# Performance work log

Measured on AMD Instinct MI355X. Metric: run time of the kernel, lower is better.

The kernel has to match this reference:

```python
import jax, jax.numpy as jnp
import numpy as np

B, S, D = 2, 1024, 1024
G, H = 8, 2
HD = D // (G * H)          # 64
E, TOPK, FF = 8, 2, 4 * D  # experts, active experts, ffn hidden
ROPE_THETA = 10000.0


def setup_inputs() -> dict:
    key = jax.random.key(0)
    ks = jax.random.split(key, 9)
    s = 0.02
    return {
        "x": jax.random.normal(ks[0], (B, S, D), jnp.float32),
        "norm1_w": jnp.ones((D,), jnp.float32),
        "Wq": jax.random.normal(ks[1], (G, D, H * HD), jnp.float32) * s,
        "Wk": jax.random.normal(ks[2], (G, D, HD), jnp.float32) * s,
        "Wv": jax.random.normal(ks[3], (G, D, HD), jnp.float32) * s,
        "norm2_w": jnp.ones((D,), jnp.float32),
        "router_w": jax.random.normal(ks[4], (D, E), jnp.float32) * s,
        "w_gate": jax.random.normal(ks[5], (E, D, FF), jnp.float32) * s,
        "w_up": jax.random.normal(ks[6], (E, D, FF), jnp.float32) * s,
        "w_down": jax.random.normal(ks[7], (E, FF, D), jnp.float32) * s,
    }


def rmsnorm(x, w, eps=1e-6):
    var = jnp.mean(x * x, axis=-1, keepdims=True)
    return w * (x * jax.lax.rsqrt(var + eps))


def rope_cos_sin(seq, hd, dtype):
    inv = 1.0 / (ROPE_THETA ** (jnp.arange(0, hd, 2, dtype=jnp.float32) / hd))
    ang = jnp.arange(seq, dtype=jnp.float32)[:, None] * inv  # [S, hd/2]
    return jnp.cos(ang).astype(dtype), jnp.sin(ang).astype(dtype)


def apply_rope(x, cos, sin):
    x1, x2 = jnp.split(x, 2, axis=-1)
    return jnp.concatenate([x1 * cos - x2 * sin, x1 * sin + x2 * cos], axis=-1)


def reference(x, norm1_w, Wq, Wk, Wv, norm2_w, router_w, w_gate, w_up, w_down):
    b, s, d = x.shape
    g, hd = Wk.shape[0], Wk.shape[-1]
    h_per_g = Wq.shape[-1] // hd
    e = router_w.shape[-1]

    # --- norm1 + grouped RoPE attention (H query heads share 1 KV per group) ---
    hx = rmsnorm(x, norm1_w)
    q = jnp.einsum('bsd,gdm->bgsm', hx, Wq).reshape(b, g, s, h_per_g, hd)
    q = q.transpose(0, 1, 3, 2, 4)                      # [b,g,h,s,hd]
    k = jnp.einsum('bsd,gde->bgse', hx, Wk)             # [b,g,s,hd]
    v = jnp.einsum('bsd,gde->bgse', hx, Wv)
    cos, sin = rope_cos_sin(s, hd, x.dtype)
    q = apply_rope(q, cos, sin)
    k = apply_rope(k, cos, sin)
    scores = jnp.einsum('bghsd,bgtd->bghst', q, k) / jnp.asarray(np.sqrt(hd), x.dtype)
    causal = jnp.tril(jnp.ones((s, s), bool))
    scores = jnp.where(causal, scores, jnp.finfo(x.dtype).min)
    attn = jax.nn.softmax(scores, axis=-1)
    o = jnp.einsum('bghst,bgtd->bghsd', attn, v)
    attn_out = o.transpose(0, 3, 1, 2, 4).reshape(b, s, d)  # concat groups, then heads
    x1 = x + attn_out

    # --- norm2 + MoE (top-k softmax router, SwiGLU experts) ---
    h2 = rmsnorm(x1, norm2_w)
    probs = jax.nn.softmax(h2 @ router_w, axis=-1)       # [b,s,E]
    topv, topi = jax.lax.top_k(probs, TOPK)
    topv = topv / jnp.sum(topv, axis=-1, keepdims=True)  # renormalize active weights
    onehot = jax.nn.one_hot(topi, e, dtype=x.dtype)      # [b,s,K,E]
    gates = jnp.einsum('bsk,bske->bse', topv, onehot)    # dense gate per expert

    moe_out = jnp.zeros_like(h2)
    for ei in range(e):  # small fixed expert count
        act = jax.nn.silu(h2 @ w_gate[ei]) * (h2 @ w_up[ei])
        moe_out = moe_out + gates[..., ei:ei + 1] * (act @ w_down[ei])

    # Switch/Mixtral load-balancing loss
    f = jnp.mean(onehot, axis=(0, 1, 2))   # fraction of assignments per expert
    p = jnp.mean(probs, axis=(0, 1))       # mean router prob per expert
    aux = jnp.asarray(e, x.dtype) * jnp.sum(f * p)

    return x1 + moe_out, aux
```

## Files before the change

### kernel.cpp

```cpp
#include <hip/hip_runtime.h>
#include <hip/hip_bf16.h>

typedef __hip_bfloat16 bf16;

#define BB 2
#define SS 1024
#define DD 1024
#define GG 8
#define HH 2
#define HDIM 64
#define EE 8
#define KTOP 2
#define FFD 4096
#define NTOK (BB*SS)
#define NSEL (NTOK*KTOP)

typedef __attribute__((ext_vector_type(8))) short bf16x8v;
typedef __attribute__((ext_vector_type(4))) float f32x4;
typedef __attribute__((ext_vector_type(4))) unsigned int u32x4;

union FragU { uint32_t u[4]; bf16x8v v; };
union FragQ { u32x4 q; bf16x8v v; };

__device__ __forceinline__ float b2f(bf16 v){ return __bfloat162float(v); }
__device__ __forceinline__ bf16  f2b(float v){ return __float2bfloat16(v); }
__device__ __forceinline__ uint32_t f2bu(float f){
  union { bf16 b; unsigned short u; } c; c.b = __float2bfloat16(f); return (uint32_t)c.u;
}
__device__ __forceinline__ uint32_t packbf(float lo, float hi){
  return f2bu(lo) | (f2bu(hi) << 16);
}

__global__ void rmsnorm_kernel(const float* __restrict__ x, const float* __restrict__ w,
                               float* __restrict__ out){
  int row = blockIdx.x, tid = threadIdx.x;
  const float* xr = x + (size_t)row * DD;
  float v0 = xr[tid];
  float v1 = xr[tid+256];
  float v2 = xr[tid+512];
  float v3 = xr[tid+768];
  float ss = v0*v0+v1*v1+v2*v2+v3*v3;
  for (int off=32; off; off>>=1) ss += __shfl_down(ss, off);
  __shared__ float red[4];
  if ((tid&63)==0) red[tid>>6]=ss;
  __syncthreads();
  float inv = rsqrtf((red[0]+red[1]+red[2]+red[3])*(1.0f/DD) + 1e-6f);
  float* orow = out + (size_t)row*DD;
  orow[tid]     = v0*inv*w[tid];
  orow[tid+256] = v1*inv*w[tid+256];
  orow[tid+512] = v2*inv*w[tid+512];
  orow[tid+768] = v3*inv*w[tid+768];
}

__global__ void rmsnorm_b16_kernel(const float* __restrict__ x, const float* __restrict__ w,
                                   bf16* __restrict__ out){
  int row = blockIdx.x, tid = threadIdx.x;
  const float* xr = x + (size_t)row * DD;
  float v0 = xr[tid];
  float v1 = xr[tid+256];
  float v2 = xr[tid+512];
  float v3 = xr[tid+768];
  float ss = v0*v0+v1*v1+v2*v2+v3*v3;
  for (int off=32; off; off>>=1) ss += __shfl_down(ss, off);
  __shared__ float red[4];
  if ((tid&63)==0) red[tid>>6]=ss;
  __syncthreads();
  float inv = rsqrtf((red[0]+red[1]+red[2]+red[3])*(1.0f/DD) + 1e-6f);
  bf16* orow = out + (size_t)row*DD;
  orow[tid]     = f2b(v0*inv*w[tid]);
  orow[tid+256] = f2b(v1*inv*w[tid+256]);
  orow[tid+512] = f2b(v2*inv*w[tid+512]);
  orow[tid+768] = f2b(v3*inv*w[tid+768]);
}

__global__ void __launch_bounds__(256) qkv_mfma(const bf16* __restrict__ hxb,
      const float* __restrict__ Wq, const float* __restrict__ Wk, const float* __restrict__ Wv,
      float* __restrict__ q, float* __restrict__ k, bf16* __restrict__ vb){
  int mtile = blockIdx.x;
  int nt = blockIdx.y;
  int g = nt >> 2, sub = nt & 3;
  const float* wsrc; int ld;
  if (sub < 2){ wsrc = Wq + (size_t)g*DD*128 + sub*64; ld = 128; }
  else if (sub == 2){ wsrc = Wk + (size_t)g*DD*64; ld = 64; }
  else { wsrc = Wv + (size_t)g*DD*64; ld = 64; }

  __shared__ __attribute__((aligned(16))) uint32_t Bt[64][20];
  int tid = threadIdx.x;
  int w = tid >> 6, l = tid & 63, lg = l >> 4, lr = l & 15;
  int wm = (w >> 1)*32, wn = (w & 1)*32;

  const bf16* arow[2];
  #pragma unroll
  for (int mf=0; mf<2; mf++)
    arow[mf] = hxb + (size_t)(mtile*64 + wm + mf*16 + lr)*DD;

  int scol = tid & 63, skp = tid >> 6;

  f32x4 acc[2][2];
  #pragma unroll
  for (int mf=0;mf<2;mf++)
    #pragma unroll
    for (int nf=0;nf<2;nf++) acc[mf][nf] = (f32x4){0,0,0,0};

  float gld[8];
  #pragma unroll
  for (int jj=0;jj<8;jj++) gld[jj] = wsrc[(size_t)(8*skp + jj)*ld + scol];

  for (int kb=0; kb<DD; kb+=32){
    __syncthreads();
    uint32_t pk[4];
    #pragma unroll
    for (int j2=0;j2<4;j2++) pk[j2] = packbf(gld[2*j2], gld[2*j2+1]);
    *(u32x4*)&Bt[scol][4*skp] = (u32x4){pk[0],pk[1],pk[2],pk[3]};
    __syncthreads();
    if (kb + 32 < DD){
      #pragma unroll
      for (int jj=0;jj<8;jj++) gld[jj] = wsrc[(size_t)(kb + 32 + 8*skp + jj)*ld + scol];
    }
    bf16x8v af[2];
    #pragma unroll
    for (int mf=0;mf<2;mf++)
      af[mf] = *(const bf16x8v*)(arow[mf] + kb + lg*8);
    #pragma unroll
    for (int nf=0;nf<2;nf++){
      FragQ bfr;
      bfr.q = *(const u32x4*)&Bt[wn + nf*16 + lr][lg*4];
      #pragma unroll
      for (int mf=0;mf<2;mf++)
        acc[mf][nf] = __builtin_amdgcn_mfma_f32_16x16x32_bf16(af[mf], bfr.v, acc[mf][nf], 0,0,0);
    }
  }
  #pragma unroll
  for (int mf=0;mf<2;mf++){
    #pragma unroll
    for (int nf=0;nf<2;nf++){
      #pragma unroll
      for (int r=0;r<4;r++){
        int token = mtile*64 + wm + mf*16 + lg*4 + r;
        int b = token >> 10, s = token & (SS-1);
        int c = wn + nf*16 + lr;
        float val = acc[mf][nf][r];
        if (sub < 2)       q[(((size_t)(b*GG+g)*HH + sub)*SS + s)*HDIM + c] = val;
        else if (sub == 2) k[(((size_t)(b*GG+g))*SS + s)*HDIM + c] = val;
        else               vb[(((size_t)(b*GG+g))*SS + s)*HDIM + c] = f2b(val);
      }
    }
  }
}

__global__ void rope_cast_kernel(const float* __restrict__ pin, bf16* __restrict__ pout, int nrows){
  int idx = blockIdx.x*256 + threadIdx.x;
  if (idx >= nrows*32) return;
  int r = idx >> 5, i = idx & 31;
  int s = r & (SS-1);
  float inv = expf(-9.210340371976184f * (float)i / 32.0f);
  float ang = (float)s * inv;
  float sn = sinf(ang), cs = cosf(ang);
  const float* row = pin + (size_t)r * HDIM;
  float a = row[i], b = row[i+32];
  pout[(size_t)r*HDIM + i]      = f2b(a*cs - b*sn);
  pout[(size_t)r*HDIM + i + 32] = f2b(a*sn + b*cs);
}

__global__ void __launch_bounds__(256) attn_mfma(
    const bf16* __restrict__ qb, const bf16* __restrict__ kb, const bf16* __restrict__ vb,
    const float* __restrict__ x, float* __restrict__ x1){
  int qt = blockIdx.x;
  int bh = blockIdx.y;
  int b = bh >> 4, gh = bh & 15;
  int bg = b*GG + (gh >> 1);
  int q0 = qt * 64;

  int tid = threadIdx.x;
  int w = tid >> 6, l = tid & 63, lg = l >> 4, lr = l & 15;

  __shared__ uint32_t Vp[32][68];
  __shared__ uint32_t Plu[4][16][33];

  const bf16* qbase = qb + ((size_t)bh*SS + q0 + w*16 + lr)*HDIM;
  bf16x8v qfr[2];
  qfr[0] = *(const bf16x8v*)(qbase + lg*8);
  qfr[1] = *(const bf16x8v*)(qbase + 32 + lg*8);

  f32x4 O[4];
  #pragma unroll
  for (int i=0;i<4;i++) O[i] = (f32x4){0,0,0,0};
  float mrow[4] = {-3e38f,-3e38f,-3e38f,-3e38f};
  float lrow[4] = {0.f,0.f,0.f,0.f};

  const bf16* kbg = kb + (size_t)bg*SS*HDIM;
  const unsigned short* vbg = (const unsigned short*)(vb + (size_t)bg*SS*HDIM);

  int c44 = (tid & 15)*4;
  int kpq = tid >> 4;

  for (int t=0; t<=qt; t++){
    int kv0 = t*64;
    __syncthreads();
    #pragma unroll
    for (int it=0; it<2; it++){
      int kp = kpq + it*16;
      const unsigned short* r0 = vbg + (size_t)(kv0 + 2*kp)*HDIM + c44;
      ushort4 a = *(const ushort4*)r0;
      ushort4 bq = *(const ushort4*)(r0 + HDIM);
      Vp[kp][c44+0] = (uint32_t)a.x | ((uint32_t)bq.x<<16);
      Vp[kp][c44+1] = (uint32_t)a.y | ((uint32_t)bq.y<<16);
      Vp[kp][c44+2] = (uint32_t)a.z | ((uint32_t)bq.z<<16);
      Vp[kp][c44+3] = (uint32_t)a.w | ((uint32_t)bq.w<<16);
    }
    __syncthreads();

    f32x4 sacc[4];
    #pragma unroll
    for (int nf=0;nf<4;nf++){
      sacc[nf] = (f32x4){0,0,0,0};
      const bf16* kr = kbg + (size_t)(kv0 + nf*16 + lr)*HDIM + lg*8;
      bf16x8v kf0 = *(const bf16x8v*)kr;
      bf16x8v kf1 = *(const bf16x8v*)(kr + 32);
      sacc[nf] = __builtin_amdgcn_mfma_f32_16x16x32_bf16(qfr[0], kf0, sacc[nf], 0,0,0);
      sacc[nf] = __builtin_amdgcn_mfma_f32_16x16x32_bf16(qfr[1], kf1, sacc[nf], 0,0,0);
    }

    bool diag = (t == qt);
    float p[4][4];
    float rmax[4] = {-3e38f,-3e38f,-3e38f,-3e38f};
    #pragma unroll
    for (int nf=0;nf<4;nf++){
      #pragma unroll
      for (int r=0;r<4;r++){
        float s = sacc[nf][r]*0.125f;
        if (diag && (nf*16+lr > w*16+lg*4+r)) s = -3e38f;
        p[nf][r] = s;
        rmax[r] = fmaxf(rmax[r], s);
      }
    }
    #pragma unroll
    for (int r=0;r<4;r++){
      #pragma unroll
      for (int mm=1; mm<16; mm<<=1) rmax[r] = fmaxf(rmax[r], __shfl_xor(rmax[r], mm));
      float mn = fmaxf(mrow[r], rmax[r]);
      float resc = __expf(mrow[r]-mn);
      mrow[r] = mn;
      float rsum = 0.f;
      #pragma unroll
      for (int nf=0;nf<4;nf++){
        float e = __expf(p[nf][r]-mn);
        p[nf][r] = e;
        rsum += e;
      }
      #pragma unroll
      for (int mm=1; mm<16; mm<<=1) rsum += __shfl_xor(rsum, mm);
      lrow[r] = lrow[r]*resc + rsum;
      O[0][r]*=resc; O[1][r]*=resc; O[2][r]*=resc; O[3][r]*=resc;
    }

    #pragma unroll
    for (int nf=0;nf<4;nf++){
      #pragma unroll
      for (int r=0;r<4;r++){
        float pnbr = __shfl_xor(p[nf][r], 1);
        if ((lr & 1) == 0)
          Plu[w][lg*4+r][(nf*16+lr)>>1] = packbf(p[nf][r], pnbr);
      }
    }

    #pragma unroll
    for (int kc=0;kc<2;kc++){
      FragU pa;
      #pragma unroll
      for (int jp=0;jp<4;jp++)
        pa.u[jp] = Plu[w][lr][kc*16 + lg*4 + jp];
      #pragma unroll
      for (int nf=0;nf<4;nf++){
        FragU vf;
        #pragma unroll
        for (int jp=0;jp<4;jp++) vf.u[jp] = Vp[kc*16 + lg*4 + jp][nf*16 + lr];
        O[nf] = __builtin_amdgcn_mfma_f32_16x16x32_bf16(pa.v, vf.v, O[nf], 0,0,0);
      }
    }
  }

  #pragma unroll
  for (int r=0;r<4;r++){
    int s = q0 + w*16 + lg*4 + r;
    float inv = 1.f/fmaxf(lrow[r], 1e-30f);
    size_t rowo = ((size_t)(b*SS + s))*DD + gh*HDIM;
    #pragma unroll
    for (int nf=0;nf<4;nf++){
      size_t oi = rowo + nf*16 + lr;
      x1[oi] = x[oi] + O[nf][r]*inv;
    }
  }
}

__global__ void router_kernel(const float* __restrict__ h2, const float* __restrict__ rw,
                              int* __restrict__ topi, float* __restrict__ topv,
                              float* __restrict__ probs){
  int token = blockIdx.x, tid = threadIdx.x;
  const float* hr = h2 + (size_t)token * DD;
  float part[EE];
  #pragma unroll
  for (int e=0;e<EE;e++) part[e]=0.f;
  for (int d = tid; d < DD; d += 256) {
    float hv = hr[d];
    #pragma unroll
    for (int e=0;e<EE;e++) part[e] += hv * rw[d*EE+e];
  }
  #pragma unroll
  for (int e=0;e<EE;e++)
    for (int off=32; off; off>>=1) part[e] += __shfl_down(part[e], off);
  __shared__ float red[4][EE];
  if ((tid&63)==0){
    #pragma unroll
    for (int e=0;e<EE;e++) red[tid>>6][e]=part[e];
  }
  __syncthreads();
  if (tid==0){
    float lg[EE];
    #pragma unroll
    for (int e=0;e<EE;e++) lg[e]=red[0][e]+red[1][e]+red[2][e]+red[3][e];
    float m = lg[0];
    #pragma unroll
    for (int e=1;e<EE;e++) m = fmaxf(m, lg[e]);
    float ex[EE], ssum=0.f;
    #pragma unroll
    for (int e=0;e<EE;e++){ ex[e]=expf(lg[e]-m); ssum+=ex[e]; }
    float p[EE];
    #pragma unroll
    for (int e=0;e<EE;e++){ p[e]=ex[e]/ssum; probs[token*EE+e]=p[e]; }
    int i1=0;
    for (int e=1;e<EE;e++) if (p[e]>p[i1]) i1=e;
    int i2=-1;
    for (int e=0;e<EE;e++) if (e!=i1 && (i2<0 || p[e]>p[i2])) i2=e;
    float g1=p[i1], g2=p[i2], gs=g1+g2;
    topi[token*2]=i1; topi[token*2+1]=i2;
    topv[token*2]=g1/gs; topv[token*2+1]=g2/gs;
  }
}

__global__ void stats_kernel(const float* __restrict__ probs, const int* __restrict__ topi,
                             float* __restrict__ sumP, int* __restrict__ counts){
  int tid = threadIdx.x;
  float ls[EE];
  int lc[EE];
  #pragma unroll
  for (int e=0;e<EE;e++){ ls[e]=0.f; lc[e]=0; }
  for (int t = tid; t < NTOK; t += 256){
    const float* pr = probs + (size_t)t*EE;
    #pragma unroll
    for (int e=0;e<EE;e++) ls[e] += pr[e];
    lc[topi[2*t]]++;
    lc[topi[2*t+1]]++;
  }
  #pragma unroll
  for (int e=0;e<EE;e++){
    for (int off=32; off; off>>=1){
      ls[e] += __shfl_down(ls[e], off);
      lc[e] += __shfl_down(lc[e], off);
    }
  }
  __shared__ float rs[4][EE];
  __shared__ int   rc[4][EE];
  if ((tid&63)==0){
    #pragma unroll
    for (int e=0;e<EE;e++){ rs[tid>>6][e]=ls[e]; rc[tid>>6][e]=lc[e]; }
  }
  __syncthreads();
  if (tid==0){
    #pragma unroll
    for (int e=0;e<EE;e++){
      sumP[e]   = rs[0][e]+rs[1][e]+rs[2][e]+rs[3][e];
      counts[e] = rc[0][e]+rc[1][e]+rc[2][e]+rc[3][e];
    }
  }
}

__global__ void fill_kernel(const int* __restrict__ topi, const float* __restrict__ topv,
                            const int* __restrict__ counts, int* __restrict__ offs,
                            int* __restrict__ tok_list, float* __restrict__ gate_list,
                            int* __restrict__ tdesc, int* __restrict__ ndesc){
  int tid = threadIdx.x;
  int w = tid >> 6, lane = tid & 63;
  if (tid < EE){
    int o = 0;
    for (int e=0;e<tid;e++) o += counts[e];
    offs[tid] = o;
  }
  if (tid == 0){
    int n = 0;
    for (int e=0;e<EE;e++){
      int t = (counts[e] + 255) >> 8;
      for (int m=0;m<t;m++) tdesc[n++] = e | (m << 8);
    }
    *ndesc = n;
  }
  int pos = 0;
  for (int e=0;e<w;e++) pos += counts[e];
  for (int j0=0; j0<NSEL; j0+=64){
    int j = j0 + lane;
    bool hit = (topi[j] == w);
    unsigned long long mask = __ballot(hit);
    if (hit){
      int idx = pos + __popcll(mask & ((1ull<<lane)-1ull));
      tok_list[idx] = j >> 1;
      gate_list[idx] = topv[j];
    }
    pos += __popcll(mask);
  }
}

__global__ void gather_kernel(const float* __restrict__ h2, const int* __restrict__ tok_list,
                              bf16* __restrict__ Abuf){
  int i = blockIdx.x*256 + threadIdx.x;
  int pos = i >> 10, d = i & 1023;
  int tok = tok_list[pos];
  Abuf[(size_t)pos*DD + d] = f2b(h2[(size_t)tok*DD + d]);
}

__global__ void __launch_bounds__(256, 2) moeA_mfma(const bf16* __restrict__ Abuf,
                            const float* __restrict__ wg, const float* __restrict__ wu,
                            bf16* __restrict__ hidden,
                            const int* __restrict__ counts, const int* __restrict__ offs,
                            const int* __restrict__ tdesc, const int* __restrict__ ndesc){
  int ti = blockIdx.y;
  if (ti >= *ndesc) return;
  int d = tdesc[ti];
  int e = d & 255, mtile = d >> 8;
  int cnt = counts[e];
  int ntile = blockIdx.x;
  int offs_e = offs[e];
  int ncol0 = ntile*64;

  __shared__ __attribute__((aligned(16))) uint32_t Bg[64][20];
  __shared__ __attribute__((aligned(16))) uint32_t Bu[64][20];

  int tid = threadIdx.x;
  int w = tid >> 6, l = tid & 63, lg = l >> 4, lr = l & 15;
  int wm = w*64;

  const bf16* arow[4];
  #pragma unroll
  for (int mf=0; mf<4; mf++){
    int slot = mtile*256 + wm + mf*16 + lr;
    if (slot >= cnt) slot = cnt - 1;
    arow[mf] = Abuf + (size_t)(offs_e + slot)*DD;
  }

  const float* wgb = wg + (size_t)e*DD*FFD + ncol0;
  const float* wub = wu + (size_t)e*DD*FFD + ncol0;
  int skp = tid >> 4;
  int scol4 = (tid & 15) * 4;

  f32x4 acc_g[4][4], acc_u[4][4];
  #pragma unroll
  for (int mf=0; mf<4; mf++)
    #pragma unroll
    for (int nf=0; nf<4; nf++){ acc_g[mf][nf] = (f32x4){0,0,0,0}; acc_u[mf][nf] = (f32x4){0,0,0,0}; }

  float4 ga0, ga1, ua0, ua1;
  ga0 = *(const float4*)&wgb[(size_t)(2*skp)*FFD + scol4];
  ga1 = *(const float4*)&wgb[(size_t)(2*skp+1)*FFD + scol4];
  ua0 = *(const float4*)&wub[(size_t)(2*skp)*FFD + scol4];
  ua1 = *(const float4*)&wub[(size_t)(2*skp+1)*FFD + scol4];

  for (int kb=0; kb<DD; kb+=32){
    __syncthreads();
    Bg[scol4+0][skp] = packbf(ga0.x, ga1.x);
    Bg[scol4+1][skp] = packbf(ga0.y, ga1.y);
    Bg[scol4+2][skp] = packbf(ga0.z, ga1.z);
    Bg[scol4+3][skp] = packbf(ga0.w, ga1.w);
    Bu[scol4+0][skp] = packbf(ua0.x, ua1.x);
    Bu[scol4+1][skp] = packbf(ua0.y, ua1.y);
    Bu[scol4+2][skp] = packbf(ua0.z, ua1.z);
    Bu[scol4+3][skp] = packbf(ua0.w, ua1.w);
    __syncthreads();
    if (kb + 32 < DD){
      ga0 = *(const float4*)&wgb[(size_t)(kb + 32 + 2*skp)*FFD + scol4];
      ga1 = *(const float4*)&wgb[(size_t)(kb + 32 + 2*skp+1)*FFD + scol4];
      ua0 = *(const float4*)&wub[(size_t)(kb + 32 + 2*skp)*FFD + scol4];
      ua1 = *(const float4*)&wub[(size_t)(kb + 32 + 2*skp+1)*FFD + scol4];
    }
    bf16x8v afr[4];
    #pragma unroll
    for (int mf=0; mf<4; mf++)
      afr[mf] = *(const bf16x8v*)(arow[mf] + kb + lg*8);
    #pragma unroll
    for (int nf=0; nf<4; nf++){
      int col = nf*16 + lr;
      FragQ fg, fu;
      fg.q = *(const u32x4*)&Bg[col][lg*4];
      fu.q = *(const u32x4*)&Bu[col][lg*4];
      #pragma unroll
      for (int mf=0; mf<4; mf++){
        acc_g[mf][nf] = __builtin_amdgcn_mfma_f32_16x16x32_bf16(afr[mf], fg.v, acc_g[mf][nf], 0,0,0);
        acc_u[mf][nf] = __builtin_amdgcn_mfma_f32_16x16x32_bf16(afr[mf], fu.v, acc_u[mf][nf], 0,0,0);
      }
    }
  }
  #pragma unroll
  for (int mf=0; mf<4; mf++){
    #pragma unroll
    for (int ri=0; ri<4; ri++){
      int slot = mtile*256 + wm + mf*16 + lg*4 + ri;
      if (slot < cnt){
        bf16* hrow = hidden + (size_t)(offs_e + slot)*FFD + ncol0;
        #pragma unroll
        for (int nf=0; nf<4; nf++){
          float gv = acc_g[mf][nf][ri];
          float uv = acc_u[mf][nf][ri];
          float act = gv / (1.f + expf(-gv)) * uv;
          hrow[nf*16 + lr] = f2b(act);
        }
      }
    }
  }
}

__global__ void __launch_bounds__(256, 2) moeB_mfma(const bf16* __restrict__ hidden,
                            const float* __restrict__ wd, float* __restrict__ moe_out,
                            const int* __restrict__ counts, const int* __restrict__ offs,
                            const int* __restrict__ tok_list, const float* __restrict__ gate_list,
                            const int* __restrict__ tdesc, const int* __restrict__ ndesc){
  int ti = blockIdx.y;
  if (ti >= *ndesc) return;
  int d = tdesc[ti];
  int e = d & 255, mtile = d >> 8;
  int cnt = counts[e];
  int ntile = blockIdx.x & 7;
  int kchunk = blockIdx.x >> 3;
  int offs_e = offs[e];
  int ncol0 = ntile*128;
  int kb0 = kchunk*1024;

  __shared__ __attribute__((aligned(16))) uint32_t Bd[128][20];

  int tid = threadIdx.x;
  int w = tid >> 6, l = tid & 63, lg = l >> 4, lr = l & 15;
  int wm = w*64;

  const bf16* arow[4];
  #pragma unroll
  for (int mf=0; mf<4; mf++){
    int slot = mtile*256 + wm + mf*16 + lr;
    if (slot >= cnt) slot = cnt - 1;
    arow[mf] = hidden + (size_t)(offs_e + slot)*FFD + kb0;
  }

  const float* wdb = wd + (size_t)e*FFD*DD + (size_t)kb0*DD + ncol0;
  int skp8 = tid >> 5;
  int scol4 = (tid & 31) * 4;

  f32x4 acc[4][8];
  #pragma unroll
  for (int mf=0; mf<4; mf++)
    #pragma unroll
    for (int nf=0; nf<8; nf++) acc[mf][nf] = (f32x4){0,0,0,0};

  float4 da0, da1, db0, db1;
  da0 = *(const float4*)&wdb[(size_t)(2*skp8)*DD + scol4];
  da1 = *(const float4*)&wdb[(size_t)(2*skp8+1)*DD + scol4];
  db0 = *(const float4*)&wdb[(size_t)(2*skp8+16)*DD + scol4];
  db1 = *(const float4*)&wdb[(size_t)(2*skp8+17)*DD + scol4];

  for (int kb=0; kb<1024; kb+=32){
    __syncthreads();
    Bd[scol4+0][skp8]   = packbf(da0.x, da1.x);
    Bd[scol4+1][skp8]   = packbf(da0.y, da1.y);
    Bd[scol4+2][skp8]   = packbf(da0.z, da1.z);
    Bd[scol4+3][skp8]   = packbf(da0.w, da1.w);
    Bd[scol4+0][skp8+8] = packbf(db0.x, db1.x);
    Bd[scol4+1][skp8+8] = packbf(db0.y, db1.y);
    Bd[scol4+2][skp8+8] = packbf(db0.z, db1.z);
    Bd[scol4+3][skp8+8] = packbf(db0.w, db1.w);
    __syncthreads();
    if (kb + 32 < 1024){
      da0 = *(const float4*)&wdb[(size_t)(kb + 32 + 2*skp8)*DD + scol4];
      da1 = *(const float4*)&wdb[(size_t)(kb + 32 + 2*skp8+1)*DD + scol4];
      db0 = *(const float4*)&wdb[(size_t)(kb + 32 + 2*skp8+16)*DD + scol4];
      db1 = *(const float4*)&wdb[(size_t)(kb + 32 + 2*skp8+17)*DD + scol4];
    }
    bf16x8v afr[4];
    #pragma unroll
    for (int mf=0; mf<4; mf++)
      afr[mf] = *(const bf16x8v*)(arow[mf] + kb + lg*8);
    #pragma unroll
    for (int nf=0; nf<8; nf++){
      int col = nf*16 + lr;
      FragQ fd;
      fd.q = *(const u32x4*)&Bd[col][lg*4];
      #pragma unroll
      for (int mf=0; mf<4; mf++)
        acc[mf][nf] = __builtin_amdgcn_mfma_f32_16x16x32_bf16(afr[mf], fd.v, acc[mf][nf], 0,0,0);
    }
  }
  #pragma unroll
  for (int mf=0; mf<4; mf++){
    #pragma unroll
    for (int ri=0; ri<4; ri++){
      int slot = mtile*256 + wm + mf*16 + lg*4 + ri;
      if (slot < cnt){
        int pos = offs_e + slot;
        int tok = tok_list[pos];
        float gate = gate_list[pos];
        float* orow = moe_out + (size_t)tok*DD + ncol0;
        #pragma unroll
        for (int nf=0; nf<8; nf++)
          atomicAdd(&orow[nf*16 + lr], gate * acc[mf][nf][ri]);
      }
    }
  }
}

__global__ void final_kernel(const float* __restrict__ x1, const float* __restrict__ moe,
                             float* __restrict__ out,
                             const int* __restrict__ counts, const float* __restrict__ sumP){
  int i = blockIdx.x*256 + threadIdx.x;
  if (i < BB*SS*DD) {
    out[i] = x1[i] + moe[i];
  } else if (i == BB*SS*DD) {
    float aux = 0.f;
    for (int e=0;e<EE;e++)
      aux += ((float)counts[e] / (float)(BB*SS*KTOP)) * (sumP[e] / (float)(BB*SS));
    out[i] = aux * (float)EE;
  }
}

extern "C" void kernel_launch(void* const* d_in, const int* in_sizes, int n_in,
                              void* d_out, int out_size, void* d_ws, size_t ws_size,
                              hipStream_t stream) {
  const float* x        = (const float*)d_in[0];
  const float* norm1_w  = (const float*)d_in[1];
  const float* Wq       = (const float*)d_in[2];
  const float* Wk       = (const float*)d_in[3];
  const float* Wv       = (const float*)d_in[4];
  const float* norm2_w  = (const float*)d_in[5];
  const float* router_w = (const float*)d_in[6];
  const float* w_gate   = (const float*)d_in[7];
  const float* w_up     = (const float*)d_in[8];
  const float* w_down   = (const float*)d_in[9];
  float* out = (float*)d_out;

  float* ws = (float*)d_ws;
  bf16*  hxb     = (bf16*)ws;
  float* qf      = ws + 1048576;
  float* kf      = ws + 3145728;
  bf16*  qbb     = (bf16*)(ws + 4194304);
  bf16*  kbb     = (bf16*)(ws + 5242880);
  bf16*  vbb     = (bf16*)(ws + 5767168);
  float* x1      = ws + 6291456;
  float* h2      = ws + 8388608;
  float* moe_out = ws + 10485760;
  int*   counts  = (int*)(ws + 12582912);
  float* sumP    = ws + 12582920;
  int*   offs    = (int*)(ws + 12582928);
  int*   topi    = (int*)(ws + 12582944);
  float* topv    = ws + 12587040;
  int*   tok_list= (int*)(ws + 12591136);
  float* gate_list = ws + 12595232;
  bf16*  hidden  = (bf16*)(ws + 12599328);
  bf16*  Abuf    = (bf16*)ws;
  int*   tdesc   = (int*)(ws + 3145728);
  int*   ndesc   = (int*)(ws + 3145728 + 24);
  float* probs   = ws + 3145728 + 32;

  hipMemsetAsync(moe_out, 0, (size_t)BB*SS*DD*sizeof(float), stream);

  rmsnorm_b16_kernel<<<NTOK, 256, 0, stream>>>(x, norm1_w, hxb);
  qkv_mfma<<<dim3(32, 32), 256, 0, stream>>>(hxb, Wq, Wk, Wv, qf, kf, vbb);
  rope_cast_kernel<<<(BB*GG*HH*SS*32)/256, 256, 0, stream>>>(qf, qbb, BB*GG*HH*SS);
  rope_cast_kernel<<<(BB*GG*SS*32)/256, 256, 0, stream>>>(kf, kbb, BB*GG*SS);
  attn_mfma<<<dim3(SS/64, BB*GG*HH), 256, 0, stream>>>(qbb, kbb, vbb, x, x1);
  rmsnorm_kernel<<<NTOK, 256, 0, stream>>>(x1, norm2_w, h2);
  router_kernel<<<NTOK, 256, 0, stream>>>(h2, router_w, topi, topv, probs);
  stats_kernel<<<1, 256, 0, stream>>>(probs, topi, sumP, counts);
  fill_kernel<<<1, 512, 0, stream>>>(topi, topv, counts, offs, tok_list, gate_list, tdesc, ndesc);
  gather_kernel<<<(NSEL*DD)/256, 256, 0, stream>>>(h2, tok_list, Abuf);
  moeA_mfma<<<dim3(64, 24), 256, 0, stream>>>(Abuf, w_gate, w_up, hidden, counts, offs, tdesc, ndesc);
  moeB_mfma<<<dim3(32, 24), 256, 0, stream>>>(hidden, w_down, moe_out, counts, offs, tok_list, gate_list, tdesc, ndesc);
  final_kernel<<<(BB*SS*DD + 1 + 255)/256, 256, 0, stream>>>(x1, moe_out, out, counts, sumP);
}
```

Before: 543.4 us.

## Narrow moeA N-tile to 32 columns with 64-deep K steps and higher occupancy

The gate/up expert GEMM now uses 32-column output tiles instead of 64, doubling the grid in x, and processes K in 64-wide steps with two MFMA sub-steps per shared-memory load. Weight staging switches to scalar per-column loads across 8 rows packed into one 16-byte LDS store, and launch bounds allow 3 blocks per CU. The aim is more parallelism and fewer barriers per K. In exchange, each A fragment is reused across fewer columns, so the A rows are re-read twice as often, and the global weight loads become 4-byte scalar accesses.

```diff
diff --git a/kernel.cpp b/kernel.cpp
--- a/kernel.cpp
+++ b/kernel.cpp
@@ -417,7 +417,7 @@
   Abuf[(size_t)pos*DD + d] = f2b(h2[(size_t)tok*DD + d]);
 }
 
-__global__ void __launch_bounds__(256, 2) moeA_mfma(const bf16* __restrict__ Abuf,
+__global__ void __launch_bounds__(256, 3) moeA_mfma(const bf16* __restrict__ Abuf,
                             const float* __restrict__ wg, const float* __restrict__ wu,
                             bf16* __restrict__ hidden,
                             const int* __restrict__ counts, const int* __restrict__ offs,
@@ -429,10 +429,10 @@
   int cnt = counts[e];
   int ntile = blockIdx.x;
   int offs_e = offs[e];
-  int ncol0 = ntile*64;
-
-  __shared__ __attribute__((aligned(16))) uint32_t Bg[64][20];
-  __shared__ __attribute__((aligned(16))) uint32_t Bu[64][20];
+  int ncol0 = ntile*32;
+
+  __shared__ __attribute__((aligned(16))) uint32_t Bg[32][36];
+  __shared__ __attribute__((aligned(16))) uint32_t Bu[32][36];
 
   int tid = threadIdx.x;
   int w = tid >> 6, l = tid & 63, lg = l >> 4, lr = l & 15;
@@ -448,52 +448,58 @@
 
   const float* wgb = wg + (size_t)e*DD*FFD + ncol0;
   const float* wub = wu + (size_t)e*DD*FFD + ncol0;
-  int skp = tid >> 4;
-  int scol4 = (tid & 15) * 4;
-
-  f32x4 acc_g[4][4], acc_u[4][4];
+  int scol = tid & 31, skp4 = tid >> 5;
+
+  f32x4 acc_g[4][2], acc_u[4][2];
   #pragma unroll
   for (int mf=0; mf<4; mf++)
     #pragma unroll
-    for (int nf=0; nf<4; nf++){ acc_g[mf][nf] = (f32x4){0,0,0,0}; acc_u[mf][nf] = (f32x4){0,0,0,0}; }
-
-  float4 ga0, ga1, ua0, ua1;
-  ga0 = *(const float4*)&wgb[(size_t)(2*skp)*FFD + scol4];
-  ga1 = *(const float4*)&wgb[(size_t)(2*skp+1)*FFD + scol4];
-  ua0 = *(const float4*)&wub[(size_t)(2*skp)*FFD + scol4];
-  ua1 = *(const float4*)&wub[(size_t)(2*skp+1)*FFD + scol4];
-
-  for (int kb=0; kb<DD; kb+=32){
-    __syncthreads();
-    Bg[scol4+0][skp] = packbf(ga0.x, ga1.x);
-    Bg[scol4+1][skp] = packbf(ga0.y, ga1.y);
-    Bg[scol4+2][skp] = packbf(ga0.z, ga1.z);
-    Bg[scol4+3][skp] = packbf(ga0.w, ga1.w);
-    Bu[scol4+0][skp] = packbf(ua0.x, ua1.x);
-    Bu[scol4+1][skp] = packbf(ua0.y, ua1.y);
-    Bu[scol4+2][skp] = packbf(ua0.z, ua1.z);
-    Bu[scol4+3][skp] = packbf(ua0.w, ua1.w);
-    __syncthreads();
-    if (kb + 32 < DD){
-      ga0 = *(const float4*)&wgb[(size_t)(kb + 32 + 2*skp)*FFD + scol4];
-      ga1 = *(const float4*)&wgb[(size_t)(kb + 32 + 2*skp+1)*FFD + scol4];
-      ua0 = *(const float4*)&wub[(size_t)(kb + 32 + 2*skp)*FFD + scol4];
-      ua1 = *(const float4*)&wub[(size_t)(kb + 32 + 2*skp+1)*FFD + scol4];
-    }
-    bf16x8v afr[4];
-    #pragma unroll
-    for (int mf=0; mf<4; mf++)
-      afr[mf] = *(const bf16x8v*)(arow[mf] + kb + lg*8);
-    #pragma unroll
-    for (int nf=0; nf<4; nf++){
-      int col = nf*16 + lr;
-      FragQ fg, fu;
-      fg.q = *(const u32x4*)&Bg[col][lg*4];
-      fu.q = *(const u32x4*)&Bu[col][lg*4];
-      #pragma unroll
-      for (int mf=0; mf<4; mf++){
-        acc_g[mf][nf] = __builtin_amdgcn_mfma_f32_16x16x32_bf16(afr[mf], fg.v, acc_g[mf][nf], 0,0,0);
-        acc_u[mf][nf] = __builtin_amdgcn_mfma_f32_16x16x32_bf16(afr[mf], fu.v, acc_u[mf][nf], 0,0,0);
+    for (int nf=0; nf<2; nf++){ acc_g[mf][nf] = (f32x4){0,0,0,0}; acc_u[mf][nf] = (f32x4){0,0,0,0}; }
+
+  float gld[8], uld[8];
+  #pragma unroll
+  for (int jj=0;jj<8;jj++){
+    gld[jj] = wgb[(size_t)(8*skp4 + jj)*FFD + scol];
+    uld[jj] = wub[(size_t)(8*skp4 + jj)*FFD + scol];
+  }
+
+  for (int kb=0; kb<DD; kb+=64){
+    __syncthreads();
+    {
+      uint32_t pg[4], pu[4];
+      #pragma unroll
+      for (int j2=0;j2<4;j2++){
+        pg[j2] = packbf(gld[2*j2], gld[2*j2+1]);
+        pu[j2] = packbf(uld[2*j2], uld[2*j2+1]);
+      }
+      *(u32x4*)&Bg[scol][4*skp4] = (u32x4){pg[0],pg[1],pg[2],pg[3]};
+      *(u32x4*)&Bu[scol][4*skp4] = (u32x4){pu[0],pu[1],pu[2],pu[3]};
+    }
+    __syncthreads();
+    if (kb + 64 < DD){
+      #pragma unroll
+      for (int jj=0;jj<8;jj++){
+        gld[jj] = wgb[(size_t)(kb + 64 + 8*skp4 + jj)*FFD + scol];
+        uld[jj] = wub[(size_t)(kb + 64 + 8*skp4 + jj)*FFD + scol];
+      }
+    }
+    #pragma unroll
+    for (int h=0; h<2; h++){
+      bf16x8v afr[4];
+      #pragma unroll
+      for (int mf=0; mf<4; mf++)
+        afr[mf] = *(const bf16x8v*)(arow[mf] + kb + h*32 + lg*8);
+      #pragma unroll
+      for (int nf=0; nf<2; nf++){
+        int col = nf*16 + lr;
+        FragQ fg, fu;
+        fg.q = *(const u32x4*)&Bg[col][h*16 + lg*4];
+        fu.q = *(const u32x4*)&Bu[col][h*16 + lg*4];
+        #pragma unroll
+        for (int mf=0; mf<4; mf++){
+          acc_g[mf][nf] = __builtin_amdgcn_mfma_f32_16x16x32_bf16(afr[mf], fg.v, acc_g[mf][nf], 0,0,0);
+          acc_u[mf][nf] = __builtin_amdgcn_mfma_f32_16x16x32_bf16(afr[mf], fu.v, acc_u[mf][nf], 0,0,0);
+        }
       }
     }
   }
@@ -505,7 +511,7 @@
       if (slot < cnt){
         bf16* hrow = hidden + (size_t)(offs_e + slot)*FFD + ncol0;
         #pragma unroll
-        for (int nf=0; nf<4; nf++){
+        for (int nf=0; nf<2; nf++){
           float gv = acc_g[mf][nf][ri];
           float uv = acc_u[mf][nf][ri];
           float act = gv / (1.f + expf(-gv)) * uv;
@@ -675,7 +681,7 @@
   stats_kernel<<<1, 256, 0, stream>>>(probs, topi, sumP, counts);
   fill_kernel<<<1, 512, 0, stream>>>(topi, topv, counts, offs, tok_list, gate_list, tdesc, ndesc);
   gather_kernel<<<(NSEL*DD)/256, 256, 0, stream>>>(h2, tok_list, Abuf);
-  moeA_mfma<<<dim3(64, 24), 256, 0, stream>>>(Abuf, w_gate, w_up, hidden, counts, offs, tdesc, ndesc);
+  moeA_mfma<<<dim3(128, 24), 256, 0, stream>>>(Abuf, w_gate, w_up, hidden, counts, offs, tdesc, ndesc);
   moeB_mfma<<<dim3(32, 24), 256, 0, stream>>>(hidden, w_down, moe_out, counts, offs, tok_list, gate_list, tdesc, ndesc);
   final_kernel<<<(BB*SS*DD + 1 + 255)/256, 256, 0, stream>>>(x1, moe_out, out, counts, sumP);
 }
```

Measured after the change: 562.4 us. 1.04x slower.
